# Kernel optimization log

Hardware: AMD Instinct MI355X
Metric: run time of the kernel (lower is better)

Reference implementation:

```python
import jax, jax.numpy as jnp
import numpy as np

B, T, S, D, H, DH = 2, 2048, 2048, 1024, 16, 64
LN_EPS = 1e-5


def setup_inputs() -> dict:
    key = jax.random.key(0)
    ks = jax.random.split(key, 8)
    return {
        "x": jax.random.normal(ks[0], (B, T, D), jnp.float32),
        "context": jax.random.normal(ks[1], (B, S, D), jnp.float32),
        "lookup_table": jax.random.normal(ks[2], (2 * T - 1, DH), jnp.float32),
        "Wq": jax.random.normal(ks[3], (D, H * DH), jnp.float32) * 0.02,
        "Wk": jax.random.normal(ks[4], (D, H * DH), jnp.float32) * 0.02,
        "Wv": jax.random.normal(ks[5], (D, H * DH), jnp.float32) * 0.02,
        "Wo": jax.random.normal(ks[6], (H * DH, D), jnp.float32) * 0.02,
        "bo": jnp.zeros((D,), jnp.float32),
        "gamma": jnp.ones((D,), jnp.float32),
        "beta": jnp.zeros((D,), jnp.float32),
    }


def skew(QE):
    # QE: [B, H, T, 2T-1] -> [B, H, T, T] via pad/reshape relative-position trick
    b, h, t, _ = QE.shape
    QE = jnp.pad(QE, ((0, 0), (0, 0), (0, 0), (0, 1))).reshape(b, h, -1)
    QE = jnp.pad(QE, ((0, 0), (0, 0), (0, t - 1))).reshape(b, h, t + 1, 2 * t - 1)
    return QE[:, :, :t, -t:]


def reference(x, context, lookup_table, Wq, Wk, Wv, Wo, bo, gamma, beta):
    scale = 1.0 / jnp.sqrt(jnp.asarray(DH, x.dtype))
    # pre-layernorm on queries
    mu = jnp.mean(x, axis=-1, keepdims=True)
    var = jnp.var(x, axis=-1, keepdims=True)
    xn = (x - mu) / jnp.sqrt(var + LN_EPS) * gamma + beta
    q = (xn @ Wq).reshape(B, T, H, DH).transpose(0, 2, 1, 3)       # [B,H,T,DH]
    k = (context @ Wk).reshape(B, S, H, DH).transpose(0, 2, 1, 3)  # [B,H,S,DH]
    v = (context @ Wv).reshape(B, S, H, DH).transpose(0, 2, 1, 3)  # [B,H,S,DH]
    score = jnp.einsum("bhtd,bhsd->bhts", q, k) * scale            # [B,H,T,S]
    rel = skew(jnp.einsum("bhtd,ld->bhtl", q, lookup_table))       # [B,H,T,T]
    # NOTE: faithful to original — QK^T gets scaled twice, rel term once
    score = (score + rel) * scale
    attn = jax.nn.softmax(score, axis=-1)
    out = jnp.einsum("bhts,bhsd->bhtd", attn, v)
    out = out.transpose(0, 2, 1, 3).reshape(B, T, H * DH)
    out = out @ Wo + bo
    # dropout=0 (eval); residual uses the layernormed x (as in source)
    return xn + out
```

## Files before the change

kernel.cpp:

```cpp
#include <hip/hip_runtime.h>

#define DEVFN __device__ __forceinline__

typedef __bf16 bf16x8 __attribute__((ext_vector_type(8)));
typedef float f32x4 __attribute__((ext_vector_type(4)));
typedef unsigned short u16;


DEVFN u16 f2bf(float f) {
  unsigned u = __builtin_bit_cast(unsigned, f);
  u += 0x7FFFu + ((u >> 16) & 1u);
  return (u16)(u >> 16);
}

DEVFN float bfbits(unsigned hi) {
  return __builtin_bit_cast(float, hi);
}

DEVFN f32x4 mfma16(bf16x8 a, bf16x8 b, f32x4 c) {
  return __builtin_amdgcn_mfma_f32_16x16x32_bf16(a, b, c, 0, 0, 0);
}

DEVFN void gl16(const u16* g, u16* l) {
  __builtin_amdgcn_global_load_lds(
      (const __attribute__((address_space(1))) unsigned int*)g,
      (__attribute__((address_space(3))) unsigned int*)l, 16, 0, 0);
}

__global__ __launch_bounds__(256) void ln_kernel(const float* __restrict__ x,
                                                 const float* __restrict__ gamma,
                                                 const float* __restrict__ beta,
                                                 float* __restrict__ xn,
                                                 u16* __restrict__ xnb) {
  int row = blockIdx.x;
  int tid = threadIdx.x;
  const float4* xr = (const float4*)(x + (size_t)row * 1024);
  float4 v = xr[tid];
  float s = v.x + v.y + v.z + v.w;
  float q = v.x * v.x + v.y * v.y + v.z * v.z + v.w * v.w;
#pragma unroll
  for (int m = 1; m < 64; m <<= 1) {
    s += __shfl_xor(s, m);
    q += __shfl_xor(q, m);
  }
  __shared__ float rs[4], rq[4];
  int w = tid >> 6;
  if ((tid & 63) == 0) { rs[w] = s; rq[w] = q; }
  __syncthreads();
  s = rs[0] + rs[1] + rs[2] + rs[3];
  q = rq[0] + rq[1] + rq[2] + rq[3];
  float mean = s * (1.0f / 1024.0f);
  float var = q * (1.0f / 1024.0f) - mean * mean;
  float inv = rsqrtf(var + 1e-5f);
  float4 g = ((const float4*)gamma)[tid];
  float4 bt = ((const float4*)beta)[tid];
  float4 o;
  o.x = (v.x - mean) * inv * g.x + bt.x;
  o.y = (v.y - mean) * inv * g.y + bt.y;
  o.z = (v.z - mean) * inv * g.z + bt.z;
  o.w = (v.w - mean) * inv * g.w + bt.w;
  ((float4*)(xn + (size_t)row * 1024))[tid] = o;
  ushort4 ob;
  ob.x = f2bf(o.x); ob.y = f2bf(o.y); ob.z = f2bf(o.z); ob.w = f2bf(o.w);
  ((ushort4*)(xnb + (size_t)row * 1024))[tid] = ob;
}

__global__ __launch_bounds__(256) void cvt2_kernel(const float* __restrict__ a,
                                                   u16* __restrict__ oa,
                                                   const float* __restrict__ bsrc,
                                                   u16* __restrict__ ob) {
  int blk = blockIdx.x;
  if (blk < 4096) {
    int i = blk * 256 + threadIdx.x;
    float4 v = ((const float4*)a)[i];
    ushort4 o;
    o.x = f2bf(v.x); o.y = f2bf(v.y); o.z = f2bf(v.z); o.w = f2bf(v.w);
    ((ushort4*)oa)[i] = o;
  } else {
    int i = (blk - 4096) * 256 + threadIdx.x;
    if (i < 65520) {
      float4 v = ((const float4*)bsrc)[i];
      ushort4 o;
      o.x = f2bf(v.x); o.y = f2bf(v.y); o.z = f2bf(v.z); o.w = f2bf(v.w);
      ((ushort4*)ob)[i] = o;
    }
  }
}

__global__ __launch_bounds__(256) void transW_kernel(const float* __restrict__ W0,
                                                     const float* __restrict__ W1,
                                                     const float* __restrict__ W2,
                                                     const float* __restrict__ W3,
                                                     u16* __restrict__ Wall) {
  __shared__ float tile[32][33];
  int z = blockIdx.z;
  const float* W = (z == 0) ? W0 : (z == 1) ? W1 : (z == 2) ? W2 : W3;
  float scale = (z == 0) ? 0.18033688011112042f : (z == 1) ? 0.125f : 1.0f;
  u16* Wt = Wall + (size_t)z * 1048576;
  int tx = threadIdx.x, ty = threadIdx.y;
  int x = blockIdx.x * 32 + tx;
  int y0 = blockIdx.y * 32;
#pragma unroll
  for (int j = 0; j < 32; j += 8)
    tile[ty + j][tx] = W[(size_t)(y0 + ty + j) * 1024 + x];
  __syncthreads();
#pragma unroll
  for (int j = 0; j < 32; j += 8)
    Wt[(size_t)(blockIdx.x * 32 + ty + j) * 1024 + y0 + tx] = f2bf(tile[tx][ty + j] * scale);
}

DEVFN void gemm_core(const u16* __restrict__ A, const u16* __restrict__ Bt,
                     u16* Ab, u16* Bb, int row0, int n0, int tid,
                     f32x4 (&acc)[2][4]) {
  int lane = tid & 63, wv = tid >> 6;
  int l16 = lane & 15, lhi = lane >> 4;
  int r8 = lane >> 3, c8 = lane & 7;
  int cx = ((c8 ^ r8) << 3);
  int swz = (l16 & 7) << 3;

  auto stage = [&](int k0) {
#pragma unroll
    for (int i = 0; i < 4; ++i) {
      int rowb = wv * 32 + i * 8;
      gl16(&A[(size_t)(row0 + rowb + r8) * 1024 + k0 + cx], &Ab[rowb * 64]);
    }
#pragma unroll
    for (int i = 0; i < 2; ++i) {
      int rowb = wv * 16 + i * 8;
      gl16(&Bt[(size_t)(n0 + rowb + r8) * 1024 + k0 + cx], &Bb[rowb * 64]);
    }
  };

  stage(0);
  asm volatile("s_waitcnt vmcnt(0)" ::: "memory");
  __syncthreads();
  for (int kk = 0; kk < 16; ++kk) {
    __builtin_amdgcn_s_setprio(1);
#pragma unroll
    for (int ks = 0; ks < 2; ++ks) {
      bf16x8 af[2], bfr[4];
#pragma unroll
      for (int mi = 0; mi < 2; ++mi) {
        int row = wv * 32 + mi * 16 + l16;
        af[mi] = *(const bf16x8*)&Ab[row * 64 + ((ks * 32 + lhi * 8) ^ swz)];
      }
#pragma unroll
      for (int ni = 0; ni < 4; ++ni) {
        int row = ni * 16 + l16;
        bfr[ni] = *(const bf16x8*)&Bb[row * 64 + ((ks * 32 + lhi * 8) ^ swz)];
      }
#pragma unroll
      for (int mi = 0; mi < 2; ++mi)
#pragma unroll
        for (int ni = 0; ni < 4; ++ni)
          acc[mi][ni] = mfma16(af[mi], bfr[ni], acc[mi][ni]);
    }
    __builtin_amdgcn_s_setprio(0);
    if (kk < 15) {
      __syncthreads();
      stage((kk + 1) * 64);
      asm volatile("s_waitcnt vmcnt(0)" ::: "memory");
      __syncthreads();
    }
  }
}

__global__ __launch_bounds__(256, 4) void qkv_kernel(const u16* __restrict__ xnb,
                                                     const u16* __restrict__ ctxb,
                                                     const u16* __restrict__ Wall,
                                                     u16* __restrict__ qb,
                                                     u16* __restrict__ kb,
                                                     u16* __restrict__ vtb) {
  __shared__ __align__(16) u16 Ab[128 * 64];
  __shared__ __align__(16) u16 Bb[64 * 64];
  int z = blockIdx.z;
  const u16* A = (z == 0) ? xnb : ctxb;
  const u16* Bt = Wall + (size_t)z * 1048576;
  int row0 = blockIdx.x * 128, n0 = blockIdx.y * 64;
  f32x4 acc[2][4] = {};
  gemm_core(A, Bt, Ab, Bb, row0, n0, threadIdx.x, acc);
  int tid = threadIdx.x, lane = tid & 63, wv = tid >> 6;
  int l16 = lane & 15, lhi = lane >> 4;
  u16* qk = (z == 0) ? qb : kb;
#pragma unroll
  for (int mi = 0; mi < 2; ++mi)
#pragma unroll
    for (int ni = 0; ni < 4; ++ni)
#pragma unroll
      for (int r = 0; r < 4; ++r) {
        int m = row0 + wv * 32 + mi * 16 + lhi * 4 + r;
        int n = n0 + ni * 16 + l16;
        int b = m >> 11, t = m & 2047, h = n >> 6, dh = n & 63;
        u16 val = f2bf(acc[mi][ni][r]);
        if (z < 2) {
          qk[(size_t)((b * 16 + h) * 2048 + t) * 64 + dh] = val;
        } else {
          int t2 = (t & ~63) | ((t & 15) << 2) | ((t >> 4) & 3);
          vtb[(size_t)((b * 16 + h) * 64 + dh) * 2048 + t2] = val;
        }
      }
}

__global__ __launch_bounds__(256, 4) void oproj_kernel(const u16* __restrict__ attnb,
                                                       const u16* __restrict__ Wall,
                                                       const float* __restrict__ bias,
                                                       const float* __restrict__ resid,
                                                       float* __restrict__ outF) {
  __shared__ __align__(16) u16 Ab[128 * 64];
  __shared__ __align__(16) u16 Bb[64 * 64];
  const u16* Bt = Wall + (size_t)3 * 1048576;
  int row0 = blockIdx.x * 128, n0 = blockIdx.y * 64;
  f32x4 acc[2][4] = {};
  gemm_core(attnb, Bt, Ab, Bb, row0, n0, threadIdx.x, acc);
  int tid = threadIdx.x, lane = tid & 63, wv = tid >> 6;
  int l16 = lane & 15, lhi = lane >> 4;
#pragma unroll
  for (int mi = 0; mi < 2; ++mi)
#pragma unroll
    for (int ni = 0; ni < 4; ++ni)
#pragma unroll
      for (int r = 0; r < 4; ++r) {
        int m = row0 + wv * 32 + mi * 16 + lhi * 4 + r;
        int n = n0 + ni * 16 + l16;
        outF[(size_t)m * 1024 + n] = acc[mi][ni][r] + bias[n] + resid[(size_t)m * 1024 + n];
      }
}

__global__ __launch_bounds__(256, 4) void flash_kernel(
    const u16* __restrict__ Qg, const u16* __restrict__ Kg,
    const u16* __restrict__ Vtg, const u16* __restrict__ Lb,
    u16* __restrict__ Og) {
  constexpr int T = 2048, H = 16;
  int p = blockIdx.x;
  int bid = (p & 7) * 128 + (p >> 3);
  int qb = bid & 31, h = (bid >> 5) & 15, b = bid >> 9;
  int tid = threadIdx.x;
  int lane = tid & 63, w = tid >> 6;
  int l16 = lane & 15, lhi = lane >> 4;

  __shared__ __align__(16) u16 Klds[64 * 64];
  __shared__ __align__(16) u16 Vt[64 * 64];
  __shared__ __align__(16) u16 Llds[128 * 64];
  __shared__ __align__(16) u16 Plds[4][16 * 64];

  const u16* qbase = Qg + (size_t)(b * H + h) * T * 64;
  const u16* kbase = Kg + (size_t)(b * H + h) * T * 64;
  const u16* vtbase = Vtg + (size_t)(b * H + h) * 64 * 2048;

  int i0b = qb * 64;
  int i0w = i0b + w * 16;
  bf16x8 aq[2];
  aq[0] = *(const bf16x8*)&qbase[(i0w + l16) * 64 + lhi * 8];
  aq[1] = *(const bf16x8*)&qbase[(i0w + l16) * 64 + 32 + lhi * 8];

  f32x4 accO[4] = {};
  float mrun[4], lsum[4];
#pragma unroll
  for (int r = 0; r < 4; ++r) { mrun[r] = -1e30f; lsum[r] = 0.0f; }

  int bandbase = T - 16 - i0w;
  int ubase0 = T - 64 - i0b;
  int uoff = 48 - 16 * w;

  int r8 = lane >> 3, c8 = lane & 7;
  int cx = ((c8 ^ r8) << 3);
  int swz = (l16 & 7) << 3;

  auto stageK = [&](int j0) {
#pragma unroll
    for (int i = 0; i < 2; ++i) {
      int rowb = w * 16 + i * 8;
      gl16(&kbase[(size_t)(j0 + rowb + r8) * 64 + cx], &Klds[rowb * 64]);
    }
  };
  auto stageLnew = [&](int kt) {
#pragma unroll
    for (int i = 0; i < 2; ++i) {
      int rowb = w * 16 + i * 8;
      gl16(&Lb[(size_t)(ubase0 + kt * 64 + 128 + rowb + r8) * 64 + cx],
           &Llds[((kt & 1) * 64 + rowb) * 64]);
    }
  };
  auto stageV = [&](int j0) {
#pragma unroll
    for (int i = 0; i < 2; ++i) {
      int rowb = w * 16 + i * 8;
      gl16(&vtbase[(size_t)(rowb + r8) * 2048 + j0 + cx], &Vt[rowb * 64]);
    }
  };

  const u16* lp = Lb + (size_t)(bandbase + l16) * 64 + lhi * 8;
  f32x4 eC = {};
#pragma unroll
  for (int ks = 0; ks < 2; ++ks)
    eC = mfma16(aq[ks], *(const bf16x8*)&lp[ks * 32], eC);

  f32x4 accS[4];
  f32x4 accE[5];
  auto computeQKE = [&](int tb) {
#pragma unroll
    for (int kb = 0; kb < 4; ++kb) accS[kb] = f32x4{0.f, 0.f, 0.f, 0.f};
    accE[0] = eC;
#pragma unroll
    for (int c = 1; c < 5; ++c) accE[c] = f32x4{0.f, 0.f, 0.f, 0.f};
    __builtin_amdgcn_s_setprio(1);
#pragma unroll
    for (int ks = 0; ks < 2; ++ks) {
#pragma unroll
      for (int kb = 0; kb < 4; ++kb) {
        int row = kb * 16 + l16;
        bf16x8 bk = *(const bf16x8*)&Klds[row * 64 + ((ks * 32 + lhi * 8) ^ swz)];
        accS[kb] = mfma16(aq[ks], bk, accS[kb]);
      }
#pragma unroll
      for (int c = 1; c < 5; ++c) {
        int ulog = uoff + c * 16;
        int prow = ((((ulog >> 6) + tb) & 1) << 6) | ((ulog & 63) + l16);
        bf16x8 bl = *(const bf16x8*)&Llds[prow * 64 + ((ks * 32 + lhi * 8) ^ swz)];
        accE[c] = mfma16(aq[ks], bl, accE[c]);
      }
    }
    __builtin_amdgcn_s_setprio(0);
    eC = accE[4];
  };

  const float THR = 11.541560327111707f;

  stageK(0);
#pragma unroll
  for (int i = 0; i < 4; ++i) {
    int rowb = w * 32 + i * 8;
    gl16(&Lb[(size_t)(ubase0 + rowb + r8) * 64 + cx], &Llds[rowb * 64]);
  }
  asm volatile("s_waitcnt vmcnt(0)" ::: "memory");
  __syncthreads();
  stageV(0);
  computeQKE(0);

  for (int kt = 0; kt < 32; ++kt) {
    __syncthreads();
    if (kt < 31) {
      stageK((kt + 1) * 64);
      stageLnew(kt);
    }
    __builtin_amdgcn_sched_barrier(0);

    float sc[4][4];
    float lm[4];
    bool need = false;
#pragma unroll
    for (int r = 0; r < 4; ++r) {
      int m = lhi * 4 + r;
      int srcl = lhi * 16 + ((l16 - m + 15) & 15);
      bool lo = (l16 <= m);
      unsigned q01, q23;
      asm("v_cvt_pk_bf16_f32 %0, %1, %2" : "=v"(q01) : "v"(accE[0][r]), "v"(accE[1][r]));
      asm("v_cvt_pk_bf16_f32 %0, %1, %2" : "=v"(q23) : "v"(accE[2][r]), "v"(accE[3][r]));
      q01 = (unsigned)__shfl((int)q01, srcl);
      q23 = (unsigned)__shfl((int)q23, srcl);
      float e4 = __shfl(accE[4][r], srcl);
      float e0 = bfbits(q01 << 16), e1 = bfbits(q01 & 0xffff0000u);
      float e2 = bfbits(q23 << 16), e3 = bfbits(q23 & 0xffff0000u);
      sc[r][0] = accS[0][r] + (lo ? e0 : e1);
      sc[r][1] = accS[1][r] + (lo ? e1 : e2);
      sc[r][2] = accS[2][r] + (lo ? e2 : e3);
      sc[r][3] = accS[3][r] + (lo ? e3 : e4);
      lm[r] = fmaxf(fmaxf(sc[r][0], sc[r][1]), fmaxf(sc[r][2], sc[r][3]));
      need |= (lm[r] > mrun[r] + THR);
    }
    if (__ballot(need)) {
#pragma unroll
      for (int r = 0; r < 4; ++r) {
        float tm = lm[r];
        tm = fmaxf(tm, __shfl_xor(tm, 1));
        tm = fmaxf(tm, __shfl_xor(tm, 2));
        tm = fmaxf(tm, __shfl_xor(tm, 4));
        tm = fmaxf(tm, __shfl_xor(tm, 8));
        float mnew = fmaxf(mrun[r], tm);
        float al = exp2f(mrun[r] - mnew);
        mrun[r] = mnew;
        lsum[r] *= al;
#pragma unroll
        for (int dt = 0; dt < 4; ++dt) accO[dt][r] *= al;
      }
    }
#pragma unroll
    for (int r = 0; r < 4; ++r) {
      int m = lhi * 4 + r;
      float mm = mrun[r];
      float pv0 = exp2f(sc[r][0] - mm);
      float pv1 = exp2f(sc[r][1] - mm);
      float pv2 = exp2f(sc[r][2] - mm);
      float pv3 = exp2f(sc[r][3] - mm);
      lsum[r] += (pv0 + pv1) + (pv2 + pv3);
      unsigned pk01, pk23;
      asm("v_cvt_pk_bf16_f32 %0, %1, %2" : "=v"(pk01) : "v"(pv0), "v"(pv1));
      asm("v_cvt_pk_bf16_f32 %0, %1, %2" : "=v"(pk23) : "v"(pv2), "v"(pv3));
      uint2 pw;
      pw.x = pk01;
      pw.y = pk23;
      *(uint2*)&Plds[w][m * 64 + ((l16 * 4) ^ ((m & 7) << 3))] = pw;
    }

    __builtin_amdgcn_s_setprio(1);
#pragma unroll
    for (int ks = 0; ks < 2; ++ks) {
      bf16x8 ap = *(const bf16x8*)&Plds[w][l16 * 64 + ((ks * 32 + lhi * 8) ^ swz)];
#pragma unroll
      for (int dt = 0; dt < 4; ++dt) {
        int row = dt * 16 + l16;
        bf16x8 bv = *(const bf16x8*)&Vt[row * 64 + ((ks * 32 + lhi * 8) ^ swz)];
        accO[dt] = mfma16(ap, bv, accO[dt]);
      }
    }
    __builtin_amdgcn_s_setprio(0);

    __syncthreads();
    if (kt < 31) {
      stageV((kt + 1) * 64);
      __builtin_amdgcn_sched_barrier(0);
      computeQKE((kt + 1) & 1);
    }
  }

#pragma unroll
  for (int r = 0; r < 4; ++r) {
    float l = lsum[r];
    l += __shfl_xor(l, 1);
    l += __shfl_xor(l, 2);
    l += __shfl_xor(l, 4);
    l += __shfl_xor(l, 8);
    lsum[r] = 1.0f / l;
  }
#pragma unroll
  for (int dt = 0; dt < 4; ++dt)
#pragma unroll
    for (int r = 0; r < 4; ++r) {
      int i = i0w + lhi * 4 + r;
      int col = h * 64 + dt * 16 + l16;
      Og[(size_t)(b * T + i) * 1024 + col] = f2bf(accO[dt][r] * lsum[r]);
    }
}

extern "C" void kernel_launch(void* const* d_in, const int* in_sizes, int n_in,
                              void* d_out, int out_size, void* d_ws, size_t ws_size,
                              hipStream_t stream) {
  const float* x = (const float*)d_in[0];
  const float* ctx = (const float*)d_in[1];
  const float* Ltab = (const float*)d_in[2];
  const float* Wq = (const float*)d_in[3];
  const float* Wk = (const float*)d_in[4];
  const float* Wv = (const float*)d_in[5];
  const float* Wo = (const float*)d_in[6];
  const float* bo = (const float*)d_in[7];
  const float* gamma = (const float*)d_in[8];
  const float* beta = (const float*)d_in[9];
  float* out = (float*)d_out;

  size_t off = 0;
  auto take = [&](size_t bytes) {
    void* p = (char*)d_ws + off;
    off += (bytes + 255) & ~(size_t)255;
    return p;
  };
  u16* xnb = (u16*)take(8388608);
  u16* ctxb = (u16*)take(8388608);
  u16* Lb = (u16*)take(4095 * 64 * 2);
  u16* Wall = (u16*)take(4 * 2097152);
  u16* qbuf = (u16*)take(8388608);
  u16* kbuf = (u16*)take(8388608);
  u16* vtbuf = (u16*)take(8388608);
  u16* attnb = (u16*)take(8388608);

  ln_kernel<<<dim3(4096), dim3(256), 0, stream>>>(x, gamma, beta, out, xnb);
  cvt2_kernel<<<dim3(4096 + 256), dim3(256), 0, stream>>>(ctx, ctxb, Ltab, Lb);
  transW_kernel<<<dim3(32, 32, 4), dim3(32, 8), 0, stream>>>(Wq, Wk, Wv, Wo, Wall);
  qkv_kernel<<<dim3(32, 16, 3), dim3(256), 0, stream>>>(xnb, ctxb, Wall, qbuf, kbuf, vtbuf);
  flash_kernel<<<dim3(1024), dim3(256), 0, stream>>>(qbuf, kbuf, vtbuf, Lb, attnb);
  oproj_kernel<<<dim3(32, 16), dim3(256), 0, stream>>>(attnb, Wall, bo, out, out);
}
```

Before: 190.9 us.

## Split QKV projection, fuse K and V GEMMs sharing context tile, simplify flash indexing

```diff
diff --git a/kernel.cpp b/kernel.cpp
--- a/kernel.cpp
+++ b/kernel.cpp
@@ -165,23 +165,16 @@
   }
 }
 
-__global__ __launch_bounds__(256, 4) void qkv_kernel(const u16* __restrict__ xnb,
-                                                     const u16* __restrict__ ctxb,
-                                                     const u16* __restrict__ Wall,
-                                                     u16* __restrict__ qb,
-                                                     u16* __restrict__ kb,
-                                                     u16* __restrict__ vtb) {
+__global__ __launch_bounds__(256, 4) void qproj_kernel(const u16* __restrict__ xnb,
+                                                       const u16* __restrict__ Wall,
+                                                       u16* __restrict__ qb) {
   __shared__ __align__(16) u16 Ab[128 * 64];
   __shared__ __align__(16) u16 Bb[64 * 64];
-  int z = blockIdx.z;
-  const u16* A = (z == 0) ? xnb : ctxb;
-  const u16* Bt = Wall + (size_t)z * 1048576;
   int row0 = blockIdx.x * 128, n0 = blockIdx.y * 64;
   f32x4 acc[2][4] = {};
-  gemm_core(A, Bt, Ab, Bb, row0, n0, threadIdx.x, acc);
+  gemm_core(xnb, Wall, Ab, Bb, row0, n0, threadIdx.x, acc);
   int tid = threadIdx.x, lane = tid & 63, wv = tid >> 6;
   int l16 = lane & 15, lhi = lane >> 4;
-  u16* qk = (z == 0) ? qb : kb;
 #pragma unroll
   for (int mi = 0; mi < 2; ++mi)
 #pragma unroll
@@ -191,13 +184,89 @@
         int m = row0 + wv * 32 + mi * 16 + lhi * 4 + r;
         int n = n0 + ni * 16 + l16;
         int b = m >> 11, t = m & 2047, h = n >> 6, dh = n & 63;
-        u16 val = f2bf(acc[mi][ni][r]);
-        if (z < 2) {
-          qk[(size_t)((b * 16 + h) * 2048 + t) * 64 + dh] = val;
-        } else {
-          int t2 = (t & ~63) | ((t & 15) << 2) | ((t >> 4) & 3);
-          vtb[(size_t)((b * 16 + h) * 64 + dh) * 2048 + t2] = val;
-        }
+        qb[(size_t)((b * 16 + h) * 2048 + t) * 64 + dh] = f2bf(acc[mi][ni][r]);
+      }
+}
+
+__global__ __launch_bounds__(256, 4) void kv_kernel(const u16* __restrict__ ctxb,
+                                                    const u16* __restrict__ Wall,
+                                                    u16* __restrict__ kbuf,
+                                                    u16* __restrict__ vtb) {
+  __shared__ __align__(16) u16 Ab[128 * 64];
+  __shared__ __align__(16) u16 Bk[64 * 64];
+  __shared__ __align__(16) u16 Bv[64 * 64];
+  const u16* Wk = Wall + 1048576;
+  const u16* Wv = Wall + 2097152;
+  int tid = threadIdx.x;
+  int lane = tid & 63, wv = tid >> 6;
+  int l16 = lane & 15, lhi = lane >> 4;
+  int r8 = lane >> 3, c8 = lane & 7;
+  int cx = ((c8 ^ r8) << 3);
+  int swz = (l16 & 7) << 3;
+  int row0 = blockIdx.x * 128, n0 = blockIdx.y * 64;
+
+  auto stage = [&](int k0) {
+#pragma unroll
+    for (int i = 0; i < 4; ++i) {
+      int rowb = wv * 32 + i * 8;
+      gl16(&ctxb[(size_t)(row0 + rowb + r8) * 1024 + k0 + cx], &Ab[rowb * 64]);
+    }
+    {
+      int rowb = wv * 16;
+      gl16(&Wk[(size_t)(n0 + rowb + r8) * 1024 + k0 + cx], &Bk[rowb * 64]);
+      gl16(&Wk[(size_t)(n0 + rowb + 8 + r8) * 1024 + k0 + cx], &Bk[(rowb + 8) * 64]);
+      gl16(&Wv[(size_t)(n0 + rowb + r8) * 1024 + k0 + cx], &Bv[rowb * 64]);
+      gl16(&Wv[(size_t)(n0 + rowb + 8 + r8) * 1024 + k0 + cx], &Bv[(rowb + 8) * 64]);
+    }
+  };
+
+  f32x4 accK[2][4] = {};
+  f32x4 accV[2][4] = {};
+  stage(0);
+  asm volatile("s_waitcnt vmcnt(0)" ::: "memory");
+  __syncthreads();
+  for (int kk = 0; kk < 16; ++kk) {
+    __builtin_amdgcn_s_setprio(1);
+#pragma unroll
+    for (int ks = 0; ks < 2; ++ks) {
+      bf16x8 af[2];
+#pragma unroll
+      for (int mi = 0; mi < 2; ++mi) {
+        int row = wv * 32 + mi * 16 + l16;
+        af[mi] = *(const bf16x8*)&Ab[row * 64 + ((ks * 32 + lhi * 8) ^ swz)];
+      }
+#pragma unroll
+      for (int ni = 0; ni < 4; ++ni) {
+        int row = ni * 16 + l16;
+        bf16x8 bk = *(const bf16x8*)&Bk[row * 64 + ((ks * 32 + lhi * 8) ^ swz)];
+        accK[0][ni] = mfma16(af[0], bk, accK[0][ni]);
+        accK[1][ni] = mfma16(af[1], bk, accK[1][ni]);
+        bf16x8 bv = *(const bf16x8*)&Bv[row * 64 + ((ks * 32 + lhi * 8) ^ swz)];
+        accV[0][ni] = mfma16(af[0], bv, accV[0][ni]);
+        accV[1][ni] = mfma16(af[1], bv, accV[1][ni]);
+      }
+    }
+    __builtin_amdgcn_s_setprio(0);
+    if (kk < 15) {
+      __syncthreads();
+      stage((kk + 1) * 64);
+      asm volatile("s_waitcnt vmcnt(0)" ::: "memory");
+      __syncthreads();
+    }
+  }
+
+#pragma unroll
+  for (int mi = 0; mi < 2; ++mi)
+#pragma unroll
+    for (int ni = 0; ni < 4; ++ni)
+#pragma unroll
+      for (int r = 0; r < 4; ++r) {
+        int m = row0 + wv * 32 + mi * 16 + lhi * 4 + r;
+        int n = n0 + ni * 16 + l16;
+        int b = m >> 11, t = m & 2047, h = n >> 6, dh = n & 63;
+        kbuf[(size_t)((b * 16 + h) * 2048 + t) * 64 + dh] = f2bf(accK[mi][ni][r]);
+        int t2 = (t & ~63) | ((t & 15) << 2) | ((t >> 4) & 3);
+        vtb[(size_t)((b * 16 + h) * 64 + dh) * 2048 + t2] = f2bf(accV[mi][ni][r]);
       }
 }
 
@@ -265,6 +334,16 @@
   int r8 = lane >> 3, c8 = lane & 7;
   int cx = ((c8 ^ r8) << 3);
   int swz = (l16 & 7) << 3;
+  int koff0 = (lhi * 8) ^ swz;
+  int koff1 = (32 + lhi * 8) ^ swz;
+  int loffrow[2][4];
+#pragma unroll
+  for (int tb = 0; tb < 2; ++tb)
+#pragma unroll
+    for (int c = 1; c < 5; ++c) {
+      int ulog = uoff + c * 16;
+      loffrow[tb][c - 1] = (((((ulog >> 6) + tb) & 1) << 6) | ((ulog & 63) + l16)) * 64;
+    }
 
   auto stageK = [&](int j0) {
 #pragma unroll
@@ -306,17 +385,15 @@
     __builtin_amdgcn_s_setprio(1);
 #pragma unroll
     for (int ks = 0; ks < 2; ++ks) {
+      int ko = ks ? koff1 : koff0;
 #pragma unroll
       for (int kb = 0; kb < 4; ++kb) {
-        int row = kb * 16 + l16;
-        bf16x8 bk = *(const bf16x8*)&Klds[row * 64 + ((ks * 32 + lhi * 8) ^ swz)];
+        bf16x8 bk = *(const bf16x8*)&Klds[(kb * 16 + l16) * 64 + ko];
         accS[kb] = mfma16(aq[ks], bk, accS[kb]);
       }
 #pragma unroll
       for (int c = 1; c < 5; ++c) {
-        int ulog = uoff + c * 16;
-        int prow = ((((ulog >> 6) + tb) & 1) << 6) | ((ulog & 63) + l16);
-        bf16x8 bl = *(const bf16x8*)&Llds[prow * 64 + ((ks * 32 + lhi * 8) ^ swz)];
+        bf16x8 bl = *(const bf16x8*)&Llds[loffrow[tb][c - 1] + ko];
         accE[c] = mfma16(aq[ks], bl, accE[c]);
       }
     }
@@ -353,18 +430,19 @@
       int m = lhi * 4 + r;
       int srcl = lhi * 16 + ((l16 - m + 15) & 15);
       bool lo = (l16 <= m);
-      unsigned q01, q23;
+      unsigned q01, q23, q45;
       asm("v_cvt_pk_bf16_f32 %0, %1, %2" : "=v"(q01) : "v"(accE[0][r]), "v"(accE[1][r]));
       asm("v_cvt_pk_bf16_f32 %0, %1, %2" : "=v"(q23) : "v"(accE[2][r]), "v"(accE[3][r]));
+      asm("v_cvt_pk_bf16_f32 %0, %1, %2" : "=v"(q45) : "v"(accE[4][r]), "v"(accE[4][r]));
       q01 = (unsigned)__shfl((int)q01, srcl);
       q23 = (unsigned)__shfl((int)q23, srcl);
-      float e4 = __shfl(accE[4][r], srcl);
-      float e0 = bfbits(q01 << 16), e1 = bfbits(q01 & 0xffff0000u);
-      float e2 = bfbits(q23 << 16), e3 = bfbits(q23 & 0xffff0000u);
-      sc[r][0] = accS[0][r] + (lo ? e0 : e1);
-      sc[r][1] = accS[1][r] + (lo ? e1 : e2);
-      sc[r][2] = accS[2][r] + (lo ? e2 : e3);
-      sc[r][3] = accS[3][r] + (lo ? e3 : e4);
+      q45 = (unsigned)__shfl((int)q45, srcl);
+      unsigned A = lo ? q01 : __builtin_amdgcn_alignbit(q23, q01, 16);
+      unsigned B = lo ? q23 : __builtin_amdgcn_alignbit(q45, q23, 16);
+      sc[r][0] = accS[0][r] + bfbits(A << 16);
+      sc[r][1] = accS[1][r] + bfbits(A & 0xffff0000u);
+      sc[r][2] = accS[2][r] + bfbits(B << 16);
+      sc[r][3] = accS[3][r] + bfbits(B & 0xffff0000u);
       lm[r] = fmaxf(fmaxf(sc[r][0], sc[r][1]), fmaxf(sc[r][2], sc[r][3]));
       need |= (lm[r] > mrun[r] + THR);
     }
@@ -405,11 +483,11 @@
     __builtin_amdgcn_s_setprio(1);
 #pragma unroll
     for (int ks = 0; ks < 2; ++ks) {
-      bf16x8 ap = *(const bf16x8*)&Plds[w][l16 * 64 + ((ks * 32 + lhi * 8) ^ swz)];
+      int ko = ks ? koff1 : koff0;
+      bf16x8 ap = *(const bf16x8*)&Plds[w][l16 * 64 + ko];
 #pragma unroll
       for (int dt = 0; dt < 4; ++dt) {
-        int row = dt * 16 + l16;
-        bf16x8 bv = *(const bf16x8*)&Vt[row * 64 + ((ks * 32 + lhi * 8) ^ swz)];
+        bf16x8 bv = *(const bf16x8*)&Vt[(dt * 16 + l16) * 64 + ko];
         accO[dt] = mfma16(ap, bv, accO[dt]);
       }
     }
@@ -475,7 +553,8 @@
   ln_kernel<<<dim3(4096), dim3(256), 0, stream>>>(x, gamma, beta, out, xnb);
   cvt2_kernel<<<dim3(4096 + 256), dim3(256), 0, stream>>>(ctx, ctxb, Ltab, Lb);
   transW_kernel<<<dim3(32, 32, 4), dim3(32, 8), 0, stream>>>(Wq, Wk, Wv, Wo, Wall);
-  qkv_kernel<<<dim3(32, 16, 3), dim3(256), 0, stream>>>(xnb, ctxb, Wall, qbuf, kbuf, vtbuf);
+  qproj_kernel<<<dim3(32, 16), dim3(256), 0, stream>>>(xnb, Wall, qbuf);
+  kv_kernel<<<dim3(32, 16), dim3(256), 0, stream>>>(ctxb, Wall, kbuf, vtbuf);
   flash_kernel<<<dim3(1024), dim3(256), 0, stream>>>(qbuf, kbuf, vtbuf, Lb, attnb);
   oproj_kernel<<<dim3(32, 16), dim3(256), 0, stream>>>(attnb, Wall, bo, out, out);
 }
```

Result: slower. 195.7 us (+2.5%).
